# Optimization experiments

Measured on AMD Instinct MI355X. Metric: run time of the kernel, lower is better.

The kernel has to match this reference:

```python
import jax, jax.numpy as jnp
import numpy as np

N, IN_F, OUT_F = 8192, 512, 128
NEG = -1e11
LRELU_SLOPE = 0.01  # torch nn.LeakyReLU default


def setup_inputs() -> dict:
    key = jax.random.key(0)
    k1, k2, k3, k4, k5 = jax.random.split(key, 5)
    h = jax.random.normal(k1, (N, IN_F), dtype=jnp.float32)
    adj = jax.random.randint(k2, (N, N), 0, 2, dtype=jnp.int32)
    # nn.Linear weights, [out, in] convention; kaiming-uniform-ish init
    w = jax.random.uniform(k3, (OUT_F, IN_F), dtype=jnp.float32,
                           minval=-1.0, maxval=1.0) / np.sqrt(IN_F)
    a1 = jax.random.uniform(k4, (1, OUT_F), dtype=jnp.float32,
                            minval=-1.0, maxval=1.0) / np.sqrt(OUT_F)
    a2 = jax.random.uniform(k5, (1, OUT_F), dtype=jnp.float32,
                            minval=-1.0, maxval=1.0) / np.sqrt(OUT_F)
    return {"h": h, "adj": adj, "w": w, "a1": a1, "a2": a2}


def reference(h, adj, w, a1, a2):
    wh = h @ w.T                                # [N, out]
    wh1 = wh @ a1.T                             # [N, 1]
    wh2 = wh @ a2.T                             # [N, 1]
    e = wh1 + wh2.T                             # [N, N] broadcast add
    e = jnp.where(e > 0, e, LRELU_SLOPE * e)    # leaky relu
    scores = jnp.where(adj > 0, e, jnp.float32(NEG))
    attention = jax.nn.softmax(scores, axis=-1)  # [N, N]
    h_new = attention @ wh                       # [N, out]
    return jax.nn.elu(h_new)
```

## Files before the change

kernel.cpp:

```cpp
#include <hip/hip_runtime.h>
#include <hip/hip_bf16.h>
#include <cstdint>
#include <cstddef>

#define NV    8192
#define KIN   512
#define MOUT  128
#define LOG2E 1.4426950408889634f

typedef __attribute__((ext_vector_type(4))) float f32x4;
typedef __attribute__((ext_vector_type(8))) short short8;

__device__ __forceinline__ float elu1(float x) { return x > 0.f ? x : expm1f(x); }

__device__ __forceinline__ unsigned int pkbf2(float a, float b) {
  union { __hip_bfloat162 h2; unsigned int u; } r;
  r.h2 = __float22bfloat162_rn(make_float2(a, b));
  return r.u;
}

__global__ __launch_bounds__(256) void k_wh(const float* __restrict__ h,
                                            const float* __restrict__ w,
                                            const float* __restrict__ a1,
                                            const float* __restrict__ a2,
                                            unsigned short* __restrict__ fragB,
                                            float* __restrict__ wh1,
                                            float* __restrict__ wh2) {
  __shared__ __align__(16) float hT[64][36];
  __shared__ __align__(16) float wT[64][128];
  const int t = threadIdx.x;
  const int row0 = blockIdx.x * 32;
  const int hr = t >> 3, hu = t & 7;
  const int wc = t >> 1, whalf = t & 1;
  const int cg = t & 31, rg = t >> 5;
  const int c0 = cg * 4, r0 = rg * 4;
  float acc[4][4] = {};

  for (int kt = 0; kt < 8; ++kt) {
    const int k0 = kt * 64;
    __syncthreads();
#pragma unroll
    for (int v = 0; v < 8; ++v)
      hT[hu + 8 * v][hr] = h[(size_t)(row0 + hr) * KIN + k0 + hu + 8 * v];
#pragma unroll
    for (int mv = 0; mv < 8; ++mv) {
      const float4 wv4 = *(const float4*)&w[(size_t)wc * KIN + k0 + whalf * 32 + mv * 4];
      wT[whalf * 32 + mv * 4 + 0][wc] = wv4.x;
      wT[whalf * 32 + mv * 4 + 1][wc] = wv4.y;
      wT[whalf * 32 + mv * 4 + 2][wc] = wv4.z;
      wT[whalf * 32 + mv * 4 + 3][wc] = wv4.w;
    }
    __syncthreads();
#pragma unroll 8
    for (int kk = 0; kk < 64; ++kk) {
      const float4 hv = *(const float4*)&hT[kk][r0];
      const float4 wv4 = *(const float4*)&wT[kk][c0];
      const float hvv[4] = {hv.x, hv.y, hv.z, hv.w};
      const float wvv[4] = {wv4.x, wv4.y, wv4.z, wv4.w};
#pragma unroll
      for (int i = 0; i < 4; ++i)
#pragma unroll
        for (int j = 0; j < 4; ++j)
          acc[i][j] = fmaf(hvv[i], wvv[j], acc[i][j]);
    }
  }

  {
    const size_t jt = (size_t)(row0 >> 6);
    const int ks = (row0 >> 5) & 1;
    const int lg = rg >> 1, ebase = (rg & 1) * 4;
    const int cgf = cg >> 2;
    const size_t fbase = (((jt * 8 + cgf) * 2 + ks) * 64 + lg * 16) * 8 + ebase;
#pragma unroll
    for (int j = 0; j < 4; ++j) {
      const int l15 = (cg & 3) * 4 + j;
      uint2 o;
      o.x = pkbf2(acc[0][j], acc[1][j]);
      o.y = pkbf2(acc[2][j], acc[3][j]);
      *(uint2*)&fragB[fbase + (size_t)l15 * 8] = o;
    }
  }

  const float4 a1v = *(const float4*)&a1[c0];
  const float4 a2v = *(const float4*)&a2[c0];
#pragma unroll
  for (int i = 0; i < 4; ++i) {
    float s1 = acc[i][0] * a1v.x + acc[i][1] * a1v.y + acc[i][2] * a1v.z + acc[i][3] * a1v.w;
    float s2 = acc[i][0] * a2v.x + acc[i][1] * a2v.y + acc[i][2] * a2v.z + acc[i][3] * a2v.w;
#pragma unroll
    for (int off = 16; off > 0; off >>= 1) {
      s1 += __shfl_down(s1, off, 32);
      s2 += __shfl_down(s2, off, 32);
    }
    if (cg == 0) {
      wh1[row0 + r0 + i] = s1 * LOG2E;
      wh2[row0 + r0 + i] = s2 * LOG2E;
    }
  }
}

__global__ __launch_bounds__(256, 4) void k_attn_p(const unsigned short* __restrict__ fragB,
                                                   const int* __restrict__ adj,
                                                   const float* __restrict__ wh1l,
                                                   const float* __restrict__ wh2l,
                                                   float* __restrict__ out_p,
                                                   float* __restrict__ psum_p,
                                                   int ntiles) {
  extern __shared__ char smem[];
  const int t = threadIdx.x;
  const int i0 = blockIdx.x * 32;
  const int jbase = blockIdx.y * ntiles * 64;
  const int lane = t & 63, wv = t >> 6;
  const int ih = wv & 1, ch = wv >> 1;
  const int l15 = lane & 15, lg = lane >> 4;
  const int mstride = ntiles * 8 + 8;

  {
    const int nchunk = ntiles >> 4;
    for (int rr = 0; rr < 8; ++rr) {
      const int r = wv * 8 + rr;
      const int* ap = adj + (size_t)(i0 + r) * NV + jbase;
      for (int c = 0; c < nchunk; ++c) {
        const int chunk = c * 64 + lane;
        const int* bp = ap + chunk * 16;
        const int4 v0 = *(const int4*)(bp);
        const int4 v1 = *(const int4*)(bp + 4);
        const int4 v2 = *(const int4*)(bp + 8);
        const int4 v3 = *(const int4*)(bp + 12);
        const unsigned int m =
            (unsigned)(v0.x & 1)        | ((unsigned)(v0.y & 1) << 1)  |
            ((unsigned)(v0.z & 1) << 2) | ((unsigned)(v0.w & 1) << 3)  |
            ((unsigned)(v1.x & 1) << 4) | ((unsigned)(v1.y & 1) << 5)  |
            ((unsigned)(v1.z & 1) << 6) | ((unsigned)(v1.w & 1) << 7)  |
            ((unsigned)(v2.x & 1) << 8) | ((unsigned)(v2.y & 1) << 9)  |
            ((unsigned)(v2.z & 1) << 10)| ((unsigned)(v2.w & 1) << 11) |
            ((unsigned)(v3.x & 1) << 12)| ((unsigned)(v3.y & 1) << 13) |
            ((unsigned)(v3.z & 1) << 14)| ((unsigned)(v3.w & 1) << 15);
        *(unsigned short*)&smem[r * mstride + chunk * 2] = (unsigned short)m;
      }
    }
  }
  __syncthreads();

  const int row = i0 + ih * 16 + l15;
  const float wh1r = wh1l[row];
  const char* mrow = smem + (ih * 16 + l15) * mstride;
  const unsigned short* bptr = fragB + (size_t)(jbase >> 6) * 8192 + ch * 4096 + lane * 8;
  const float* w2ptr = wh2l + jbase + lg * 8;

  f32x4 acc[4] = {};
  f32x4 accs = {};
  short8 onesf;
#pragma unroll
  for (int e = 0; e < 8; ++e) onesf[e] = (short)0x3F80;

  uint2 m2 = *(const uint2*)&mrow[0];
  float4 wq0 = *(const float4*)(w2ptr);
  float4 wq1 = *(const float4*)(w2ptr + 4);
  float4 wq2 = *(const float4*)(w2ptr + 32);
  float4 wq3 = *(const float4*)(w2ptr + 36);
  w2ptr += 64;
  short8 bf[8];
#pragma unroll
  for (int ks = 0; ks < 2; ++ks)
#pragma unroll
    for (int cgl = 0; cgl < 4; ++cgl)
      bf[ks * 4 + cgl] = *(const short8*)(bptr + cgl * 1024 + ks * 512);
  bptr += 8192;

  for (int it = 0; it < ntiles; ++it) {
    const unsigned int m16 = ((m2.x >> (8 * lg)) & 0xFFu) |
                             (((m2.y >> (8 * lg)) & 0xFFu) << 8);
    short8 af[2];
#pragma unroll
    for (int ks = 0; ks < 2; ++ks) {
      const float4 wa = ks ? wq2 : wq0;
      const float4 wb = ks ? wq3 : wq1;
      const float w2v[8] = {wa.x, wa.y, wa.z, wa.w, wb.x, wb.y, wb.z, wb.w};
      union { short8 s8; __hip_bfloat162 h2[4]; } pk;
#pragma unroll
      for (int e = 0; e < 4; ++e) {
        const float x0 = wh1r + w2v[2 * e];
        const float x1 = wh1r + w2v[2 * e + 1];
        const float l0 = fmaxf(x0, 0.01f * x0);
        const float l1 = fmaxf(x1, 0.01f * x1);
        float p0 = __builtin_amdgcn_exp2f(l0);
        float p1 = __builtin_amdgcn_exp2f(l1);
        p0 = ((m16 >> (ks * 8 + 2 * e)) & 1u) ? p0 : 0.f;
        p1 = ((m16 >> (ks * 8 + 2 * e + 1)) & 1u) ? p1 : 0.f;
        pk.h2[e] = __float22bfloat162_rn(make_float2(p0, p1));
      }
      af[ks] = pk.s8;
    }
    if (it + 1 < ntiles) {
      m2 = *(const uint2*)&mrow[(it + 1) * 8];
      wq0 = *(const float4*)(w2ptr);
      wq1 = *(const float4*)(w2ptr + 4);
      wq2 = *(const float4*)(w2ptr + 32);
      wq3 = *(const float4*)(w2ptr + 36);
      w2ptr += 64;
    }
    acc[0] = __builtin_amdgcn_mfma_f32_16x16x32_bf16(af[0], bf[0], acc[0], 0, 0, 0);
    acc[1] = __builtin_amdgcn_mfma_f32_16x16x32_bf16(af[0], bf[1], acc[1], 0, 0, 0);
    acc[2] = __builtin_amdgcn_mfma_f32_16x16x32_bf16(af[0], bf[2], acc[2], 0, 0, 0);
    acc[3] = __builtin_amdgcn_mfma_f32_16x16x32_bf16(af[0], bf[3], acc[3], 0, 0, 0);
    accs   = __builtin_amdgcn_mfma_f32_16x16x32_bf16(af[0], onesf, accs, 0, 0, 0);
    acc[0] = __builtin_amdgcn_mfma_f32_16x16x32_bf16(af[1], bf[4], acc[0], 0, 0, 0);
    acc[1] = __builtin_amdgcn_mfma_f32_16x16x32_bf16(af[1], bf[5], acc[1], 0, 0, 0);
    acc[2] = __builtin_amdgcn_mfma_f32_16x16x32_bf16(af[1], bf[6], acc[2], 0, 0, 0);
    acc[3] = __builtin_amdgcn_mfma_f32_16x16x32_bf16(af[1], bf[7], acc[3], 0, 0, 0);
    accs   = __builtin_amdgcn_mfma_f32_16x16x32_bf16(af[1], onesf, accs, 0, 0, 0);
    if (it + 1 < ntiles) {
#pragma unroll
      for (int ks = 0; ks < 2; ++ks)
#pragma unroll
        for (int cgl = 0; cgl < 4; ++cgl)
          bf[ks * 4 + cgl] = *(const short8*)(bptr + cgl * 1024 + ks * 512);
      bptr += 8192;
    }
  }

  if (ch == 0 && l15 == 0) {
#pragma unroll
    for (int r = 0; r < 4; ++r)
      psum_p[(size_t)blockIdx.y * NV + i0 + ih * 16 + lg * 4 + r] = accs[r];
  }

  const size_t ob = ((size_t)blockIdx.y * NV + i0 + ih * 16) * MOUT + ch * 64;
#pragma unroll
  for (int cgl = 0; cgl < 4; ++cgl)
#pragma unroll
    for (int r = 0; r < 4; ++r)
      out_p[ob + (size_t)(lg * 4 + r) * MOUT + cgl * 16 + l15] = acc[cgl][r];
}

__global__ __launch_bounds__(256) void k_comb(const float* __restrict__ out_p,
                                              const float* __restrict__ psum_p,
                                              float* __restrict__ out, int S) {
  const int idx = (blockIdx.x * 256 + threadIdx.x) * 4;
  const int n = idx >> 7;
  float denom = 0.f;
  for (int s = 0; s < S; ++s) denom += psum_p[(size_t)s * NV + n];
  float4 acc = {0.f, 0.f, 0.f, 0.f};
  for (int s = 0; s < S; ++s) {
    const float4 v = *(const float4*)&out_p[(size_t)s * NV * MOUT + idx];
    acc.x += v.x; acc.y += v.y; acc.z += v.z; acc.w += v.w;
  }
  const float inv = 1.f / denom;
  float4 o;
  o.x = elu1(acc.x * inv);
  o.y = elu1(acc.y * inv);
  o.z = elu1(acc.z * inv);
  o.w = elu1(acc.w * inv);
  *(float4*)&out[idx] = o;
}

extern "C" void kernel_launch(void* const* d_in, const int* in_sizes, int n_in,
                              void* d_out, int out_size, void* d_ws, size_t ws_size,
                              hipStream_t stream) {
  const float* h  = (const float*)d_in[0];
  const int* adj  = (const int*)d_in[1];
  const float* w  = (const float*)d_in[2];
  const float* a1 = (const float*)d_in[3];
  const float* a2 = (const float*)d_in[4];
  float* out = (float*)d_out;

  char* ws = (char*)d_ws;
  unsigned short* fragB = (unsigned short*)ws;
  size_t off = (size_t)MOUT * NV * 2;
  float* wh1 = (float*)(ws + off); off += (size_t)NV * 4;
  float* wh2 = (float*)(ws + off); off += (size_t)NV * 4;
  float* psum_p = (float*)(ws + off); off += (size_t)8 * NV * 4;
  float* out_p = (float*)(ws + off);

  int S = 8;
  while (S > 1 && off + (size_t)S * NV * MOUT * 4 > ws_size) S >>= 1;
  const int ntiles = 128 / S;
  const size_t smbytes = (size_t)32 * (ntiles * 8 + 8);

  k_wh<<<NV / 32, 256, 0, stream>>>(h, w, a1, a2, fragB, wh1, wh2);
  k_attn_p<<<dim3(NV / 32, S), 256, smbytes, stream>>>(fragB, adj, wh1, wh2, out_p, psum_p, ntiles);
  k_comb<<<(NV * MOUT / 4) / 256, 256, 0, stream>>>(out_p, psum_p, out, S);
}
```

Measured before the change: 141.6 us.

## Process 64 rows per block so each wave reuses B fragments across two row groups

Doubles the row tile of the attention kernel from 32 to 64 rows per block, so each wave computes two 16-row groups against the same loaded wh B fragments. This halves the reads of the bf16 wh fragments and of wh2 per output row, and doubles the MFMA work per B load. In exchange it uses more accumulator registers, doubles the shared-memory mask buffer, halves the grid size, and drops the software prefetch of wh2.

```diff
diff --git a/kernel.cpp b/kernel.cpp
--- a/kernel.cpp
+++ b/kernel.cpp
@@ -108,7 +108,7 @@
                                                    int ntiles) {
   extern __shared__ char smem[];
   const int t = threadIdx.x;
-  const int i0 = blockIdx.x * 32;
+  const int i0 = blockIdx.x * 64;
   const int jbase = blockIdx.y * ntiles * 64;
   const int lane = t & 63, wv = t >> 6;
   const int ih = wv & 1, ch = wv >> 1;
@@ -117,8 +117,8 @@
 
   {
     const int nchunk = ntiles >> 4;
-    for (int rr = 0; rr < 8; ++rr) {
-      const int r = wv * 8 + rr;
+    for (int rr = 0; rr < 16; ++rr) {
+      const int r = wv * 16 + rr;
       const int* ap = adj + (size_t)(i0 + r) * NV + jbase;
       for (int c = 0; c < nchunk; ++c) {
         const int chunk = c * 64 + lane;
@@ -142,24 +142,22 @@
   }
   __syncthreads();
 
-  const int row = i0 + ih * 16 + l15;
-  const float wh1r = wh1l[row];
-  const char* mrow = smem + (ih * 16 + l15) * mstride;
+  const int rb = ih * 32;
+  const float wh1a = wh1l[i0 + rb + l15];
+  const float wh1b = wh1l[i0 + rb + 16 + l15];
+  const char* mrowa = smem + (rb + l15) * mstride;
+  const char* mrowb = smem + (rb + 16 + l15) * mstride;
   const unsigned short* bptr = fragB + (size_t)(jbase >> 6) * 8192 + ch * 4096 + lane * 8;
   const float* w2ptr = wh2l + jbase + lg * 8;
 
-  f32x4 acc[4] = {};
-  f32x4 accs = {};
+  f32x4 acc[2][4] = {};
+  f32x4 accs[2] = {};
   short8 onesf;
 #pragma unroll
   for (int e = 0; e < 8; ++e) onesf[e] = (short)0x3F80;
 
-  uint2 m2 = *(const uint2*)&mrow[0];
-  float4 wq0 = *(const float4*)(w2ptr);
-  float4 wq1 = *(const float4*)(w2ptr + 4);
-  float4 wq2 = *(const float4*)(w2ptr + 32);
-  float4 wq3 = *(const float4*)(w2ptr + 36);
-  w2ptr += 64;
+  uint2 m2a = *(const uint2*)&mrowa[0];
+  uint2 m2b = *(const uint2*)&mrowb[0];
   short8 bf[8];
 #pragma unroll
   for (int ks = 0; ks < 2; ++ks)
@@ -169,47 +167,64 @@
   bptr += 8192;
 
   for (int it = 0; it < ntiles; ++it) {
-    const unsigned int m16 = ((m2.x >> (8 * lg)) & 0xFFu) |
-                             (((m2.y >> (8 * lg)) & 0xFFu) << 8);
-    short8 af[2];
+    const unsigned int m16a = ((m2a.x >> (8 * lg)) & 0xFFu) |
+                              (((m2a.y >> (8 * lg)) & 0xFFu) << 8);
+    const unsigned int m16b = ((m2b.x >> (8 * lg)) & 0xFFu) |
+                              (((m2b.y >> (8 * lg)) & 0xFFu) << 8);
+    const float4 wq0 = *(const float4*)(w2ptr);
+    const float4 wq1 = *(const float4*)(w2ptr + 4);
+    const float4 wq2 = *(const float4*)(w2ptr + 32);
+    const float4 wq3 = *(const float4*)(w2ptr + 36);
+    w2ptr += 64;
+
+    short8 afa[2], afb[2];
 #pragma unroll
     for (int ks = 0; ks < 2; ++ks) {
       const float4 wa = ks ? wq2 : wq0;
       const float4 wb = ks ? wq3 : wq1;
       const float w2v[8] = {wa.x, wa.y, wa.z, wa.w, wb.x, wb.y, wb.z, wb.w};
-      union { short8 s8; __hip_bfloat162 h2[4]; } pk;
+      union { short8 s8; unsigned int u[4]; } pka, pkb;
 #pragma unroll
       for (int e = 0; e < 4; ++e) {
-        const float x0 = wh1r + w2v[2 * e];
-        const float x1 = wh1r + w2v[2 * e + 1];
-        const float l0 = fmaxf(x0, 0.01f * x0);
-        const float l1 = fmaxf(x1, 0.01f * x1);
-        float p0 = __builtin_amdgcn_exp2f(l0);
-        float p1 = __builtin_amdgcn_exp2f(l1);
-        p0 = ((m16 >> (ks * 8 + 2 * e)) & 1u) ? p0 : 0.f;
-        p1 = ((m16 >> (ks * 8 + 2 * e + 1)) & 1u) ? p1 : 0.f;
-        pk.h2[e] = __float22bfloat162_rn(make_float2(p0, p1));
+        const float x0 = wh1a + w2v[2 * e];
+        const float x1 = wh1a + w2v[2 * e + 1];
+        const float y0 = wh1b + w2v[2 * e];
+        const float y1 = wh1b + w2v[2 * e + 1];
+        const float lx0 = fmaxf(x0, 0.01f * x0);
+        const float lx1 = fmaxf(x1, 0.01f * x1);
+        const float ly0 = fmaxf(y0, 0.01f * y0);
+        const float ly1 = fmaxf(y1, 0.01f * y1);
+        float px0 = __builtin_amdgcn_exp2f(lx0);
+        float px1 = __builtin_amdgcn_exp2f(lx1);
+        float py0 = __builtin_amdgcn_exp2f(ly0);
+        float py1 = __builtin_amdgcn_exp2f(ly1);
+        px0 = ((m16a >> (ks * 8 + 2 * e)) & 1u) ? px0 : 0.f;
+        px1 = ((m16a >> (ks * 8 + 2 * e + 1)) & 1u) ? px1 : 0.f;
+        py0 = ((m16b >> (ks * 8 + 2 * e)) & 1u) ? py0 : 0.f;
+        py1 = ((m16b >> (ks * 8 + 2 * e + 1)) & 1u) ? py1 : 0.f;
+        pka.u[e] = pkbf2(px0, px1);
+        pkb.u[e] = pkbf2(py0, py1);
       }
-      af[ks] = pk.s8;
+      afa[ks] = pka.s8;
+      afb[ks] = pkb.s8;
     }
     if (it + 1 < ntiles) {
-      m2 = *(const uint2*)&mrow[(it + 1) * 8];
-      wq0 = *(const float4*)(w2ptr);
-      wq1 = *(const float4*)(w2ptr + 4);
-      wq2 = *(const float4*)(w2ptr + 32);
-      wq3 = *(const float4*)(w2ptr + 36);
-      w2ptr += 64;
-    }
-    acc[0] = __builtin_amdgcn_mfma_f32_16x16x32_bf16(af[0], bf[0], acc[0], 0, 0, 0);
-    acc[1] = __builtin_amdgcn_mfma_f32_16x16x32_bf16(af[0], bf[1], acc[1], 0, 0, 0);
-    acc[2] = __builtin_amdgcn_mfma_f32_16x16x32_bf16(af[0], bf[2], acc[2], 0, 0, 0);
-    acc[3] = __builtin_amdgcn_mfma_f32_16x16x32_bf16(af[0], bf[3], acc[3], 0, 0, 0);
-    accs   = __builtin_amdgcn_mfma_f32_16x16x32_bf16(af[0], onesf, accs, 0, 0, 0);
-    acc[0] = __builtin_amdgcn_mfma_f32_16x16x32_bf16(af[1], bf[4], acc[0], 0, 0, 0);
-    acc[1] = __builtin_amdgcn_mfma_f32_16x16x32_bf16(af[1], bf[5], acc[1], 0, 0, 0);
-    acc[2] = __builtin_amdgcn_mfma_f32_16x16x32_bf16(af[1], bf[6], acc[2], 0, 0, 0);
-    acc[3] = __builtin_amdgcn_mfma_f32_16x16x32_bf16(af[1], bf[7], acc[3], 0, 0, 0);
-    accs   = __builtin_amdgcn_mfma_f32_16x16x32_bf16(af[1], onesf, accs, 0, 0, 0);
+      m2a = *(const uint2*)&mrowa[(it + 1) * 8];
+      m2b = *(const uint2*)&mrowb[(it + 1) * 8];
+    }
+#pragma unroll
+    for (int ks = 0; ks < 2; ++ks) {
+      acc[0][0] = __builtin_amdgcn_mfma_f32_16x16x32_bf16(afa[ks], bf[ks * 4 + 0], acc[0][0], 0, 0, 0);
+      acc[0][1] = __builtin_amdgcn_mfma_f32_16x16x32_bf16(afa[ks], bf[ks * 4 + 1], acc[0][1], 0, 0, 0);
+      acc[0][2] = __builtin_amdgcn_mfma_f32_16x16x32_bf16(afa[ks], bf[ks * 4 + 2], acc[0][2], 0, 0, 0);
+      acc[0][3] = __builtin_amdgcn_mfma_f32_16x16x32_bf16(afa[ks], bf[ks * 4 + 3], acc[0][3], 0, 0, 0);
+      accs[0]   = __builtin_amdgcn_mfma_f32_16x16x32_bf16(afa[ks], onesf, accs[0], 0, 0, 0);
+      acc[1][0] = __builtin_amdgcn_mfma_f32_16x16x32_bf16(afb[ks], bf[ks * 4 + 0], acc[1][0], 0, 0, 0);
+      acc[1][1] = __builtin_amdgcn_mfma_f32_16x16x32_bf16(afb[ks], bf[ks * 4 + 1], acc[1][1], 0, 0, 0);
+      acc[1][2] = __builtin_amdgcn_mfma_f32_16x16x32_bf16(afb[ks], bf[ks * 4 + 2], acc[1][2], 0, 0, 0);
+      acc[1][3] = __builtin_amdgcn_mfma_f32_16x16x32_bf16(afb[ks], bf[ks * 4 + 3], acc[1][3], 0, 0, 0);
+      accs[1]   = __builtin_amdgcn_mfma_f32_16x16x32_bf16(afb[ks], onesf, accs[1], 0, 0, 0);
+    }
     if (it + 1 < ntiles) {
 #pragma unroll
       for (int ks = 0; ks < 2; ++ks)
@@ -222,16 +237,21 @@
 
   if (ch == 0 && l15 == 0) {
 #pragma unroll
-    for (int r = 0; r < 4; ++r)
-      psum_p[(size_t)blockIdx.y * NV + i0 + ih * 16 + lg * 4 + r] = accs[r];
-  }
-
-  const size_t ob = ((size_t)blockIdx.y * NV + i0 + ih * 16) * MOUT + ch * 64;
-#pragma unroll
-  for (int cgl = 0; cgl < 4; ++cgl)
-#pragma unroll
-    for (int r = 0; r < 4; ++r)
-      out_p[ob + (size_t)(lg * 4 + r) * MOUT + cgl * 16 + l15] = acc[cgl][r];
+    for (int rg = 0; rg < 2; ++rg)
+#pragma unroll
+      for (int r = 0; r < 4; ++r)
+        psum_p[(size_t)blockIdx.y * NV + i0 + rb + rg * 16 + lg * 4 + r] = accs[rg][r];
+  }
+
+#pragma unroll
+  for (int rg = 0; rg < 2; ++rg) {
+    const size_t ob = ((size_t)blockIdx.y * NV + i0 + rb + rg * 16) * MOUT + ch * 64;
+#pragma unroll
+    for (int cgl = 0; cgl < 4; ++cgl)
+#pragma unroll
+      for (int r = 0; r < 4; ++r)
+        out_p[ob + (size_t)(lg * 4 + r) * MOUT + cgl * 16 + l15] = acc[rg][cgl][r];
+  }
 }
 
 __global__ __launch_bounds__(256) void k_comb(const float* __restrict__ out_p,
@@ -276,9 +296,9 @@
   int S = 8;
   while (S > 1 && off + (size_t)S * NV * MOUT * 4 > ws_size) S >>= 1;
   const int ntiles = 128 / S;
-  const size_t smbytes = (size_t)32 * (ntiles * 8 + 8);
+  const size_t smbytes = (size_t)64 * (ntiles * 8 + 8);
 
   k_wh<<<NV / 32, 256, 0, stream>>>(h, w, a1, a2, fragB, wh1, wh2);
-  k_attn_p<<<dim3(NV / 32, S), 256, smbytes, stream>>>(fragB, adj, wh1, wh2, out_p, psum_p, ntiles);
+  k_attn_p<<<dim3(NV / 64, S), 256, smbytes, stream>>>(fragB, adj, wh1, wh2, out_p, psum_p, ntiles);
   k_comb<<<(NV * MOUT / 4) / 256, 256, 0, stream>>>(out_p, psum_p, out, S);
 }
```

New measurement: 130.4 us. -8.0%, faster.

## Drop split-K partials; stream adjacency mask while computing full-row attention

Applied to the files above, without the earlier changes.

The attention kernel no longer splits the neighbour dimension into partial sums. Each block of 16 rows now covers all 8192 columns, which removes the separate combine kernel and the partial output and denominator traffic. The adjacency mask is loaded in quarter chunks, and the next chunk's global loads are interleaved with MFMA compute on the current chunk. Waves now split output columns (32 each) rather than rows, so each wave recomputes the exp values for the same 16 rows. The cost is redundant exp work across waves and a fixed grid of 512 blocks.

```diff
diff --git a/kernel.cpp b/kernel.cpp
--- a/kernel.cpp
+++ b/kernel.cpp
@@ -7,6 +7,7 @@
 #define KIN   512
 #define MOUT  128
 #define LOG2E 1.4426950408889634f
+#define MSTRIDE 1032
 
 typedef __attribute__((ext_vector_type(4))) float f32x4;
 typedef __attribute__((ext_vector_type(8))) short short8;
@@ -99,160 +100,137 @@
   }
 }
 
-__global__ __launch_bounds__(256, 4) void k_attn_p(const unsigned short* __restrict__ fragB,
-                                                   const int* __restrict__ adj,
-                                                   const float* __restrict__ wh1l,
-                                                   const float* __restrict__ wh2l,
-                                                   float* __restrict__ out_p,
-                                                   float* __restrict__ psum_p,
-                                                   int ntiles) {
-  extern __shared__ char smem[];
+__device__ __forceinline__ void issue_sub(const int* __restrict__ abase, int wv, int c,
+                                          int k, int lane, int4 (&d)[4]) {
+  const int row = wv * 4 + (k >> 1);
+  const int* p = abase + (size_t)row * NV + c * 2048 + (k & 1) * 1024 + lane * 16;
+  d[0] = *(const int4*)(p);
+  d[1] = *(const int4*)(p + 4);
+  d[2] = *(const int4*)(p + 8);
+  d[3] = *(const int4*)(p + 12);
+}
+
+__device__ __forceinline__ void write_sub(char* sm, int wv, int c, int k, int lane,
+                                          const int4 (&s)[4]) {
+  const int row = wv * 4 + (k >> 1);
+  const int tile = c * 32 + (k & 1) * 16 + (lane >> 2);
+  unsigned int us = 0;
+#pragma unroll
+  for (int m = 0; m < 4; ++m) {
+    us |= (unsigned)(s[m].x & 1) << (4 * m);
+    us |= (unsigned)(s[m].y & 1) << (4 * m + 1);
+    us |= (unsigned)(s[m].z & 1) << (4 * m + 2);
+    us |= (unsigned)(s[m].w & 1) << (4 * m + 3);
+  }
+  *(unsigned short*)&sm[row * MSTRIDE + tile * 8 + (lane & 3) * 2] = (unsigned short)us;
+}
+
+__global__ __launch_bounds__(256) void k_attn(const unsigned short* __restrict__ fragB,
+                                              const int* __restrict__ adj,
+                                              const float* __restrict__ wh1l,
+                                              const float* __restrict__ wh2l,
+                                              float* __restrict__ out) {
+  __shared__ char smask[16 * MSTRIDE];
   const int t = threadIdx.x;
-  const int i0 = blockIdx.x * 32;
-  const int jbase = blockIdx.y * ntiles * 64;
+  const int i0 = blockIdx.x * 16;
   const int lane = t & 63, wv = t >> 6;
-  const int ih = wv & 1, ch = wv >> 1;
   const int l15 = lane & 15, lg = lane >> 4;
-  const int mstride = ntiles * 8 + 8;
-
-  {
-    const int nchunk = ntiles >> 4;
-    for (int rr = 0; rr < 8; ++rr) {
-      const int r = wv * 8 + rr;
-      const int* ap = adj + (size_t)(i0 + r) * NV + jbase;
-      for (int c = 0; c < nchunk; ++c) {
-        const int chunk = c * 64 + lane;
-        const int* bp = ap + chunk * 16;
-        const int4 v0 = *(const int4*)(bp);
-        const int4 v1 = *(const int4*)(bp + 4);
-        const int4 v2 = *(const int4*)(bp + 8);
-        const int4 v3 = *(const int4*)(bp + 12);
-        const unsigned int m =
-            (unsigned)(v0.x & 1)        | ((unsigned)(v0.y & 1) << 1)  |
-            ((unsigned)(v0.z & 1) << 2) | ((unsigned)(v0.w & 1) << 3)  |
-            ((unsigned)(v1.x & 1) << 4) | ((unsigned)(v1.y & 1) << 5)  |
-            ((unsigned)(v1.z & 1) << 6) | ((unsigned)(v1.w & 1) << 7)  |
-            ((unsigned)(v2.x & 1) << 8) | ((unsigned)(v2.y & 1) << 9)  |
-            ((unsigned)(v2.z & 1) << 10)| ((unsigned)(v2.w & 1) << 11) |
-            ((unsigned)(v3.x & 1) << 12)| ((unsigned)(v3.y & 1) << 13) |
-            ((unsigned)(v3.z & 1) << 14)| ((unsigned)(v3.w & 1) << 15);
-        *(unsigned short*)&smem[r * mstride + chunk * 2] = (unsigned short)m;
+  const int* abase = adj + (size_t)i0 * NV;
+
+  int4 ga[4], gb[4];
+  issue_sub(abase, wv, 0, 0, lane, ga);
+  issue_sub(abase, wv, 0, 1, lane, gb);
+#pragma unroll
+  for (int k = 2; k < 8; ++k) {
+    if (k & 1) { write_sub(smask, wv, 0, k - 2, lane, gb); issue_sub(abase, wv, 0, k, lane, gb); }
+    else       { write_sub(smask, wv, 0, k - 2, lane, ga); issue_sub(abase, wv, 0, k, lane, ga); }
+  }
+  write_sub(smask, wv, 0, 6, lane, ga);
+  write_sub(smask, wv, 0, 7, lane, gb);
+
+  const float wh1r = wh1l[i0 + l15];
+  const char* mrow = smask + l15 * MSTRIDE;
+  const float* w2base = wh2l + lg * 8;
+  const unsigned short* bb = fragB + (size_t)(wv * 2) * 1024 + lane * 8;
+
+  f32x4 acc0 = {}, acc1 = {}, accs = {};
+  short8 onesf;
+#pragma unroll
+  for (int e = 0; e < 8; ++e) onesf[e] = (short)0x3F80;
+
+  for (int q = 0; q < 4; ++q) {
+    __syncthreads();
+#pragma unroll 4
+    for (int tt = 0; tt < 32; ++tt) {
+      const int T = q * 32 + tt;
+      if (q < 3 && (tt & 3) == 0) {
+        const int k = tt >> 2;
+        if (k & 1) {
+          if (k >= 2) write_sub(smask, wv, q + 1, k - 2, lane, gb);
+          issue_sub(abase, wv, q + 1, k, lane, gb);
+        } else {
+          if (k >= 2) write_sub(smask, wv, q + 1, k - 2, lane, ga);
+          issue_sub(abase, wv, q + 1, k, lane, ga);
+        }
       }
-    }
-  }
-  __syncthreads();
-
-  const int row = i0 + ih * 16 + l15;
-  const float wh1r = wh1l[row];
-  const char* mrow = smem + (ih * 16 + l15) * mstride;
-  const unsigned short* bptr = fragB + (size_t)(jbase >> 6) * 8192 + ch * 4096 + lane * 8;
-  const float* w2ptr = wh2l + jbase + lg * 8;
-
-  f32x4 acc[4] = {};
-  f32x4 accs = {};
-  short8 onesf;
-#pragma unroll
-  for (int e = 0; e < 8; ++e) onesf[e] = (short)0x3F80;
-
-  uint2 m2 = *(const uint2*)&mrow[0];
-  float4 wq0 = *(const float4*)(w2ptr);
-  float4 wq1 = *(const float4*)(w2ptr + 4);
-  float4 wq2 = *(const float4*)(w2ptr + 32);
-  float4 wq3 = *(const float4*)(w2ptr + 36);
-  w2ptr += 64;
-  short8 bf[8];
-#pragma unroll
-  for (int ks = 0; ks < 2; ++ks)
-#pragma unroll
-    for (int cgl = 0; cgl < 4; ++cgl)
-      bf[ks * 4 + cgl] = *(const short8*)(bptr + cgl * 1024 + ks * 512);
-  bptr += 8192;
-
-  for (int it = 0; it < ntiles; ++it) {
-    const unsigned int m16 = ((m2.x >> (8 * lg)) & 0xFFu) |
-                             (((m2.y >> (8 * lg)) & 0xFFu) << 8);
-    short8 af[2];
-#pragma unroll
-    for (int ks = 0; ks < 2; ++ks) {
-      const float4 wa = ks ? wq2 : wq0;
-      const float4 wb = ks ? wq3 : wq1;
-      const float w2v[8] = {wa.x, wa.y, wa.z, wa.w, wb.x, wb.y, wb.z, wb.w};
-      union { short8 s8; __hip_bfloat162 h2[4]; } pk;
+      const unsigned short* bp = bb + (size_t)T * 8192;
+      const short8 bf00 = *(const short8*)(bp);
+      const short8 bf01 = *(const short8*)(bp + 512);
+      const short8 bf10 = *(const short8*)(bp + 1024);
+      const short8 bf11 = *(const short8*)(bp + 1536);
+      const uint2 m2 = *(const uint2*)&mrow[T * 8];
+      const float* w2p = w2base + T * 64;
+      const float4 wq0 = *(const float4*)(w2p);
+      const float4 wq1 = *(const float4*)(w2p + 4);
+      const float4 wq2 = *(const float4*)(w2p + 32);
+      const float4 wq3 = *(const float4*)(w2p + 36);
+      const unsigned int m8a = (m2.x >> (8 * lg)) & 0xFFu;
+      const unsigned int m8b = (m2.y >> (8 * lg)) & 0xFFu;
+
+      const float wA[8] = {wq0.x, wq0.y, wq0.z, wq0.w, wq1.x, wq1.y, wq1.z, wq1.w};
+      const float wB[8] = {wq2.x, wq2.y, wq2.z, wq2.w, wq3.x, wq3.y, wq3.z, wq3.w};
+      union { short8 s8; unsigned int u[4]; } p0, p1;
 #pragma unroll
       for (int e = 0; e < 4; ++e) {
-        const float x0 = wh1r + w2v[2 * e];
-        const float x1 = wh1r + w2v[2 * e + 1];
-        const float l0 = fmaxf(x0, 0.01f * x0);
-        const float l1 = fmaxf(x1, 0.01f * x1);
-        float p0 = __builtin_amdgcn_exp2f(l0);
-        float p1 = __builtin_amdgcn_exp2f(l1);
-        p0 = ((m16 >> (ks * 8 + 2 * e)) & 1u) ? p0 : 0.f;
-        p1 = ((m16 >> (ks * 8 + 2 * e + 1)) & 1u) ? p1 : 0.f;
-        pk.h2[e] = __float22bfloat162_rn(make_float2(p0, p1));
+        float x0 = wh1r + wA[2 * e];
+        float x1 = wh1r + wA[2 * e + 1];
+        float y0 = wh1r + wB[2 * e];
+        float y1 = wh1r + wB[2 * e + 1];
+        x0 = fmaxf(x0, 0.01f * x0);
+        x1 = fmaxf(x1, 0.01f * x1);
+        y0 = fmaxf(y0, 0.01f * y0);
+        y1 = fmaxf(y1, 0.01f * y1);
+        float px0 = __builtin_amdgcn_exp2f(x0);
+        float px1 = __builtin_amdgcn_exp2f(x1);
+        float py0 = __builtin_amdgcn_exp2f(y0);
+        float py1 = __builtin_amdgcn_exp2f(y1);
+        px0 = ((m8a >> (2 * e)) & 1u) ? px0 : 0.f;
+        px1 = ((m8a >> (2 * e + 1)) & 1u) ? px1 : 0.f;
+        py0 = ((m8b >> (2 * e)) & 1u) ? py0 : 0.f;
+        py1 = ((m8b >> (2 * e + 1)) & 1u) ? py1 : 0.f;
+        p0.u[e] = pkbf2(px0, px1);
+        p1.u[e] = pkbf2(py0, py1);
       }
-      af[ks] = pk.s8;
-    }
-    if (it + 1 < ntiles) {
-      m2 = *(const uint2*)&mrow[(it + 1) * 8];
-      wq0 = *(const float4*)(w2ptr);
-      wq1 = *(const float4*)(w2ptr + 4);
-      wq2 = *(const float4*)(w2ptr + 32);
-      wq3 = *(const float4*)(w2ptr + 36);
-      w2ptr += 64;
-    }
-    acc[0] = __builtin_amdgcn_mfma_f32_16x16x32_bf16(af[0], bf[0], acc[0], 0, 0, 0);
-    acc[1] = __builtin_amdgcn_mfma_f32_16x16x32_bf16(af[0], bf[1], acc[1], 0, 0, 0);
-    acc[2] = __builtin_amdgcn_mfma_f32_16x16x32_bf16(af[0], bf[2], acc[2], 0, 0, 0);
-    acc[3] = __builtin_amdgcn_mfma_f32_16x16x32_bf16(af[0], bf[3], acc[3], 0, 0, 0);
-    accs   = __builtin_amdgcn_mfma_f32_16x16x32_bf16(af[0], onesf, accs, 0, 0, 0);
-    acc[0] = __builtin_amdgcn_mfma_f32_16x16x32_bf16(af[1], bf[4], acc[0], 0, 0, 0);
-    acc[1] = __builtin_amdgcn_mfma_f32_16x16x32_bf16(af[1], bf[5], acc[1], 0, 0, 0);
-    acc[2] = __builtin_amdgcn_mfma_f32_16x16x32_bf16(af[1], bf[6], acc[2], 0, 0, 0);
-    acc[3] = __builtin_amdgcn_mfma_f32_16x16x32_bf16(af[1], bf[7], acc[3], 0, 0, 0);
-    accs   = __builtin_amdgcn_mfma_f32_16x16x32_bf16(af[1], onesf, accs, 0, 0, 0);
-    if (it + 1 < ntiles) {
-#pragma unroll
-      for (int ks = 0; ks < 2; ++ks)
-#pragma unroll
-        for (int cgl = 0; cgl < 4; ++cgl)
-          bf[ks * 4 + cgl] = *(const short8*)(bptr + cgl * 1024 + ks * 512);
-      bptr += 8192;
-    }
-  }
-
-  if (ch == 0 && l15 == 0) {
-#pragma unroll
-    for (int r = 0; r < 4; ++r)
-      psum_p[(size_t)blockIdx.y * NV + i0 + ih * 16 + lg * 4 + r] = accs[r];
-  }
-
-  const size_t ob = ((size_t)blockIdx.y * NV + i0 + ih * 16) * MOUT + ch * 64;
-#pragma unroll
-  for (int cgl = 0; cgl < 4; ++cgl)
-#pragma unroll
-    for (int r = 0; r < 4; ++r)
-      out_p[ob + (size_t)(lg * 4 + r) * MOUT + cgl * 16 + l15] = acc[cgl][r];
-}
-
-__global__ __launch_bounds__(256) void k_comb(const float* __restrict__ out_p,
-                                              const float* __restrict__ psum_p,
-                                              float* __restrict__ out, int S) {
-  const int idx = (blockIdx.x * 256 + threadIdx.x) * 4;
-  const int n = idx >> 7;
-  float denom = 0.f;
-  for (int s = 0; s < S; ++s) denom += psum_p[(size_t)s * NV + n];
-  float4 acc = {0.f, 0.f, 0.f, 0.f};
-  for (int s = 0; s < S; ++s) {
-    const float4 v = *(const float4*)&out_p[(size_t)s * NV * MOUT + idx];
-    acc.x += v.x; acc.y += v.y; acc.z += v.z; acc.w += v.w;
-  }
-  const float inv = 1.f / denom;
-  float4 o;
-  o.x = elu1(acc.x * inv);
-  o.y = elu1(acc.y * inv);
-  o.z = elu1(acc.z * inv);
-  o.w = elu1(acc.w * inv);
-  *(float4*)&out[idx] = o;
+      acc0 = __builtin_amdgcn_mfma_f32_16x16x32_bf16(p0.s8, bf00, acc0, 0, 0, 0);
+      acc1 = __builtin_amdgcn_mfma_f32_16x16x32_bf16(p0.s8, bf10, acc1, 0, 0, 0);
+      accs = __builtin_amdgcn_mfma_f32_16x16x32_bf16(p0.s8, onesf, accs, 0, 0, 0);
+      acc0 = __builtin_amdgcn_mfma_f32_16x16x32_bf16(p1.s8, bf01, acc0, 0, 0, 0);
+      acc1 = __builtin_amdgcn_mfma_f32_16x16x32_bf16(p1.s8, bf11, acc1, 0, 0, 0);
+      accs = __builtin_amdgcn_mfma_f32_16x16x32_bf16(p1.s8, onesf, accs, 0, 0, 0);
+    }
+    if (q < 3) {
+      write_sub(smask, wv, q + 1, 6, lane, ga);
+      write_sub(smask, wv, q + 1, 7, lane, gb);
+    }
+  }
+
+#pragma unroll
+  for (int r = 0; r < 4; ++r) {
+    const float inv = 1.f / accs[r];
+    const size_t ob = (size_t)(i0 + lg * 4 + r) * MOUT + wv * 32 + l15;
+    out[ob] = elu1(acc0[r] * inv);
+    out[ob + 16] = elu1(acc1[r] * inv);
+  }
 }
 
 extern "C" void kernel_launch(void* const* d_in, const int* in_sizes, int n_in,
@@ -269,16 +247,8 @@
   unsigned short* fragB = (unsigned short*)ws;
   size_t off = (size_t)MOUT * NV * 2;
   float* wh1 = (float*)(ws + off); off += (size_t)NV * 4;
-  float* wh2 = (float*)(ws + off); off += (size_t)NV * 4;
-  float* psum_p = (float*)(ws + off); off += (size_t)8 * NV * 4;
-  float* out_p = (float*)(ws + off);
-
-  int S = 8;
-  while (S > 1 && off + (size_t)S * NV * MOUT * 4 > ws_size) S >>= 1;
-  const int ntiles = 128 / S;
-  const size_t smbytes = (size_t)32 * (ntiles * 8 + 8);
+  float* wh2 = (float*)(ws + off);
 
   k_wh<<<NV / 32, 256, 0, stream>>>(h, w, a1, a2, fragB, wh1, wh2);
-  k_attn_p<<<dim3(NV / 32, S), 256, smbytes, stream>>>(fragB, adj, wh1, wh2, out_p, psum_p, ntiles);
-  k_comb<<<(NV * MOUT / 4) / 256, 256, 0, stream>>>(out_p, psum_p, out, S);
-}
+  k_attn<<<NV / 16, 256, 0, stream>>>(fragB, adj, wh1, wh2, out);
+}
```

After: 173.1 us. +22.2%, slower.
